# Kernel tuning notes

Hardware: AMD Instinct MI355X
Metric: run time of the kernel (lower is better)

Reference implementation:

```python
import jax, jax.numpy as jnp
import numpy as np


def setup_inputs() -> dict:
    key = jax.random.key(0)
    ks = jax.random.split(key, 7)
    B, C, N, D = 32, 256, 4096, 256
    s = 0.05
    return {
        "x": jax.random.normal(ks[0], (B, C, N), dtype=jnp.float32),
        "Wq": jax.random.normal(ks[1], (D, C), dtype=jnp.float32) * s,
        "bq": jax.random.normal(ks[2], (D,), dtype=jnp.float32) * s,
        "Wk": jax.random.normal(ks[3], (D, C), dtype=jnp.float32) * s,
        "bk": jax.random.normal(ks[4], (D,), dtype=jnp.float32) * s,
        "Wv": jax.random.normal(ks[5], (D, C), dtype=jnp.float32) * s,
        "bv": jax.random.normal(ks[6], (D,), dtype=jnp.float32) * s,
    }


def reference(x, Wq, bq, Wk, bk, Wv, bv):
    # 1x1 Conv1d == per-timestep linear: [B,C,N] x [D,C] -> [B,D,N]
    Q = jnp.einsum("bcn,dc->bdn", x, Wq) + bq[None, :, None]
    K = jnp.einsum("bcn,dc->bdn", x, Wk) + bk[None, :, None]
    V = jnp.einsum("bcn,dc->bdn", x, Wv) + bv[None, :, None]
    N = x.shape[-1]
    scale = 1.0 / jnp.sqrt(jnp.asarray(N, dtype=x.dtype))
    # channel-attention: scores are [B, D, D] (Q @ K^T over the time axis)
    scores = jnp.einsum("bdn,ben->bde", Q, K) * scale
    weights = jax.nn.softmax(scores, axis=-1)
    out = jnp.einsum("bde,ben->bdn", weights, V)  # [B, D, N]
    return out
```

## Files before the change

kernel.cpp:

```cpp
#include <hip/hip_runtime.h>
#include <cstdint>
#include <cstddef>


typedef float f32x4 __attribute__((ext_vector_type(4)));
typedef __bf16 bf16x8 __attribute__((ext_vector_type(8)));
typedef unsigned short u16;
typedef u16 u16x8 __attribute__((ext_vector_type(8)));
typedef u16 u16x4 __attribute__((ext_vector_type(4)));

__device__ __forceinline__ u16 f2bf(float f) {
    unsigned u = __builtin_bit_cast(unsigned, f);
    u += 0x7FFFu + ((u >> 16) & 1u);
    return (u16)(u >> 16);
}
__device__ __forceinline__ float bf2f(u16 h) {
    unsigned u = ((unsigned)h) << 16;
    return __builtin_bit_cast(float, u);
}
__device__ __forceinline__ f32x4 mfma16(bf16x8 a, bf16x8 b, f32x4 c) {
    return __builtin_amdgcn_mfma_f32_16x16x32_bf16(a, b, c, 0, 0, 0);
}

__global__ void k_wvt(const float* __restrict__ Wv, u16* __restrict__ WvT) {
    const int eb = blockIdx.x;
    const int c  = threadIdx.x;
    u16x8 pk;
#pragma unroll
    for (int j = 0; j < 8; ++j) pk[j] = f2bf(Wv[(eb * 8 + j) * 256 + c]);
    *(u16x8*)&WvT[c * 256 + eb * 8] = pk;
}

__global__ void k_wcvt(const float* __restrict__ Wq, const float* __restrict__ Wk,
                       u16* __restrict__ Wqb, u16* __restrict__ Wkb) {
    const int m = blockIdx.x >> 5, chunk = blockIdx.x & 31;
    const float* src = m == 0 ? Wq : Wk;
    u16* dst = m == 0 ? Wqb : Wkb;
    const int i = chunk * 2048 + threadIdx.x * 8;
    f32x4 w0 = *(const f32x4*)(src + i);
    f32x4 w1 = *(const f32x4*)(src + i + 4);
    u16x8 pk;
    pk[0] = f2bf(w0[0]); pk[1] = f2bf(w0[1]); pk[2] = f2bf(w0[2]); pk[3] = f2bf(w0[3]);
    pk[4] = f2bf(w1[0]); pk[5] = f2bf(w1[1]); pk[6] = f2bf(w1[2]); pk[7] = f2bf(w1[3]);
    *(u16x8*)&dst[i] = pk;
}

__global__ __launch_bounds__(512, 2) void k_gram_b(const float* __restrict__ x,
                                                   u16* __restrict__ Gpart,
                                                   float* __restrict__ rsum) {
    __shared__ __align__(16) u16 lds[2][256 * 64];
    __shared__ float ldsr[256];
    const int b = blockIdx.x >> 3, split = blockIdx.x & 7;
    const int t = threadIdx.x;
    const int lane = t & 63, wid = t >> 6;
    const int g = lane >> 4, q = lane & 15;

    if (t < 256) ldsr[t] = 0.f;

    f32x4 zero4 = {0.f, 0.f, 0.f, 0.f};
    f32x4 acc[2][16];
#pragma unroll
    for (int i = 0; i < 2; ++i)
#pragma unroll
        for (int j = 0; j < 16; ++j) acc[i][j] = zero4;

    const int c_st = t >> 1, half = t & 1;
    const int swz_w = (c_st & 7) << 3;
    const float* xp = x + ((size_t)b * 256 + c_st) * 4096 + split * 512 + half * 32;

    float s = 0.f;
    f32x4 R[8];
#pragma unroll
    for (int j = 0; j < 8; ++j) R[j] = *(const f32x4*)(xp + j * 4);
#pragma unroll
    for (int kk = 0; kk < 4; ++kk) {
        f32x4 w0 = R[2 * kk], w1 = R[2 * kk + 1];
        s += w0[0] + w0[1] + w0[2] + w0[3] + w1[0] + w1[1] + w1[2] + w1[3];
        u16x8 pk;
        pk[0] = f2bf(w0[0]); pk[1] = f2bf(w0[1]); pk[2] = f2bf(w0[2]); pk[3] = f2bf(w0[3]);
        pk[4] = f2bf(w1[0]); pk[5] = f2bf(w1[1]); pk[6] = f2bf(w1[2]); pk[7] = f2bf(w1[3]);
        *(u16x8*)&lds[0][(c_st * 64 + half * 32 + kk * 8) ^ swz_w] = pk;
    }
    __syncthreads();

    for (int nc = 0; nc < 8; ++nc) {
        const int cur = nc & 1;
        if (nc < 7) {
#pragma unroll
            for (int j = 0; j < 8; ++j) R[j] = *(const f32x4*)(xp + (nc + 1) * 64 + j * 4);
        }
#pragma unroll
        for (int ks = 0; ks < 2; ++ks) {
            const int c0 = 32 * wid + q;
            const int c1 = c0 + 16;
            bf16x8 a0 = *(const bf16x8*)&lds[cur][(c0 * 64 + ks * 32 + g * 8) ^ ((c0 & 7) << 3)];
            bf16x8 a1 = *(const bf16x8*)&lds[cur][(c1 * 64 + ks * 32 + g * 8) ^ ((c1 & 7) << 3)];
#pragma unroll
            for (int et = 0; et < 16; ++et) {
                const int c2 = et * 16 + q;
                bf16x8 bb = *(const bf16x8*)&lds[cur][(c2 * 64 + ks * 32 + g * 8) ^ ((c2 & 7) << 3)];
                acc[0][et] = mfma16(a0, bb, acc[0][et]);
                acc[1][et] = mfma16(a1, bb, acc[1][et]);
            }
        }
        if (nc < 7) {
#pragma unroll
            for (int kk = 0; kk < 4; ++kk) {
                f32x4 w0 = R[2 * kk], w1 = R[2 * kk + 1];
                s += w0[0] + w0[1] + w0[2] + w0[3] + w1[0] + w1[1] + w1[2] + w1[3];
                u16x8 pk;
                pk[0] = f2bf(w0[0]); pk[1] = f2bf(w0[1]); pk[2] = f2bf(w0[2]); pk[3] = f2bf(w0[3]);
                pk[4] = f2bf(w1[0]); pk[5] = f2bf(w1[1]); pk[6] = f2bf(w1[2]); pk[7] = f2bf(w1[3]);
                *(u16x8*)&lds[cur ^ 1][(c_st * 64 + half * 32 + kk * 8) ^ swz_w] = pk;
            }
        }
        __syncthreads();
    }

    atomicAdd(&ldsr[c_st], s);

    u16* gp = Gpart + (size_t)(split * 32 + b) * 65536;
#pragma unroll
    for (int dt = 0; dt < 2; ++dt)
#pragma unroll
        for (int et = 0; et < 16; ++et)
#pragma unroll
            for (int rr = 0; rr < 4; ++rr) {
                const int cc = 32 * wid + dt * 16 + 4 * g + rr;
                gp[cc * 256 + et * 16 + q] = f2bf(acc[dt][et][rr]);
            }
    __syncthreads();
    if (t < 256) atomicAdd(&rsum[b * 256 + t], ldsr[t]);
}

__global__ void k_reduce_b(const u16* __restrict__ Gpart, u16* __restrict__ Gb) {
    const size_t j = ((size_t)blockIdx.x * 256 + threadIdx.x) * 8;
    float s[8];
#pragma unroll
    for (int i = 0; i < 8; ++i) s[i] = 0.f;
#pragma unroll
    for (int sp = 0; sp < 8; ++sp) {
        u16x8 v = *(const u16x8*)(Gpart + (size_t)sp * 2097152 + j);
#pragma unroll
        for (int i = 0; i < 8; ++i) s[i] += bf2f(v[i]);
    }
    u16x8 pk;
#pragma unroll
    for (int i = 0; i < 8; ++i) pk[i] = f2bf(s[i]);
    *(u16x8*)&Gb[j] = pk;
}

__global__ __launch_bounds__(512, 4) void k_T(const u16* __restrict__ Gb,
                                              const u16* __restrict__ Wkb,
                                              u16* __restrict__ Tws) {
    const int b = blockIdx.x >> 3, ebase = (blockIdx.x & 7) * 32;
    const int t = threadIdx.x;
    const int lane = t & 63, wid = t >> 6;
    const int g = lane >> 4, q = lane & 15;

    f32x4 zero4 = {0.f, 0.f, 0.f, 0.f};
    f32x4 acc[2][2];
#pragma unroll
    for (int i = 0; i < 2; ++i)
#pragma unroll
        for (int j = 0; j < 2; ++j) acc[i][j] = zero4;

    const u16* gp = Gb + (size_t)b * 65536;
#pragma unroll
    for (int ks = 0; ks < 8; ++ks) {
        bf16x8 a0 = *(const bf16x8*)&gp[(32 * wid + q) * 256 + ks * 32 + g * 8];
        bf16x8 a1 = *(const bf16x8*)&gp[(32 * wid + 16 + q) * 256 + ks * 32 + g * 8];
        bf16x8 b0 = *(const bf16x8*)&Wkb[(ebase + q) * 256 + ks * 32 + g * 8];
        bf16x8 b1 = *(const bf16x8*)&Wkb[(ebase + 16 + q) * 256 + ks * 32 + g * 8];
        acc[0][0] = mfma16(a0, b0, acc[0][0]);
        acc[0][1] = mfma16(a0, b1, acc[0][1]);
        acc[1][0] = mfma16(a1, b0, acc[1][0]);
        acc[1][1] = mfma16(a1, b1, acc[1][1]);
    }
#pragma unroll
    for (int dt = 0; dt < 2; ++dt)
#pragma unroll
        for (int etl = 0; etl < 2; ++etl) {
            const int e = ebase + etl * 16 + q;
            const int cb = 32 * wid + dt * 16 + 4 * g;
            u16x4 pk;
            pk[0] = f2bf(acc[dt][etl][0]); pk[1] = f2bf(acc[dt][etl][1]);
            pk[2] = f2bf(acc[dt][etl][2]); pk[3] = f2bf(acc[dt][etl][3]);
            *(u16x4*)&Tws[((size_t)b * 256 + e) * 256 + cb] = pk;
        }
}

__global__ __launch_bounds__(256, 2) void k_SWM(
    const u16* __restrict__ Tws, const float* __restrict__ rsum,
    const float* __restrict__ Wq, const u16* __restrict__ Wqb,
    const float* __restrict__ Wk,
    const float* __restrict__ bqv, const float* __restrict__ bkv,
    const float* __restrict__ bvv,
    const u16* __restrict__ WvT, u16* __restrict__ Mws, float* __restrict__ cpv) {
    __shared__ __align__(16) u16 Wlds[64 * 256];
    __shared__ float r_[256], v_[256], bk_[256], bv_[256], u_[64], bq_[64];
    const int b = blockIdx.x >> 2, dbase = (blockIdx.x & 3) * 64;
    const int t = threadIdx.x;
    const int lane = t & 63, wid = t >> 6;
    const int g = lane >> 4, q = lane & 15;

    r_[t] = rsum[b * 256 + t];
    bk_[t] = bkv[t];
    bv_[t] = bvv[t];
    if (t < 64) bq_[t] = bqv[dbase + t];
    __syncthreads();

    {
        float s = 0.f; const float* wp = Wk + (size_t)t * 256;
#pragma unroll 4
        for (int c = 0; c < 256; c += 4) {
            f32x4 w = *(const f32x4*)(wp + c);
            f32x4 rr = *(const f32x4*)(&r_[c]);
            s += w[0] * rr[0] + w[1] * rr[1] + w[2] * rr[2] + w[3] * rr[3];
        }
        v_[t] = s;
    }
    if (t < 64) {
        float s = 0.f; const float* wp = Wq + (size_t)(dbase + t) * 256;
#pragma unroll 4
        for (int c = 0; c < 256; c += 4) {
            f32x4 w = *(const f32x4*)(wp + c);
            f32x4 rr = *(const f32x4*)(&r_[c]);
            s += w[0] * rr[0] + w[1] * rr[1] + w[2] * rr[2] + w[3] * rr[3];
        }
        u_[t] = s;
    }
    __syncthreads();

    f32x4 zero4 = {0.f, 0.f, 0.f, 0.f};
    f32x4 acc[16];
#pragma unroll
    for (int j = 0; j < 16; ++j) acc[j] = zero4;

    const u16* tp = Tws + (size_t)b * 65536;
    const int d_l = wid * 16 + q;
#pragma unroll 2
    for (int ks = 0; ks < 8; ++ks) {
        bf16x8 bb = *(const bf16x8*)&Wqb[(dbase + d_l) * 256 + ks * 32 + g * 8];
#pragma unroll
        for (int et = 0; et < 16; ++et) {
            bf16x8 aa = *(const bf16x8*)&tp[(et * 16 + q) * 256 + ks * 32 + g * 8];
            acc[et] = mfma16(aa, bb, acc[et]);
        }
    }

    {
        const float ud = u_[d_l], bqd = bq_[d_l];
        float m = -3.4e38f;
#pragma unroll
        for (int et = 0; et < 16; ++et)
#pragma unroll
            for (int rr = 0; rr < 4; ++rr) {
                const int e = et * 16 + 4 * g + rr;
                float s = (acc[et][rr] + ud * bk_[e] + bqd * v_[e] + 4096.f * bqd * bk_[e]) * 0.015625f;
                acc[et][rr] = s;
                m = fmaxf(m, s);
            }
        m = fmaxf(m, __shfl_xor(m, 16));
        m = fmaxf(m, __shfl_xor(m, 32));
        float lsum = 0.f;
#pragma unroll
        for (int et = 0; et < 16; ++et)
#pragma unroll
            for (int rr = 0; rr < 4; ++rr) {
                float p = __expf(acc[et][rr] - m);
                acc[et][rr] = p;
                lsum += p;
            }
        lsum += __shfl_xor(lsum, 16);
        lsum += __shfl_xor(lsum, 32);
        const float inv = 1.f / lsum;
        float cp = 0.f;
#pragma unroll
        for (int et = 0; et < 16; ++et)
#pragma unroll
            for (int rr = 0; rr < 4; ++rr) {
                const int e = et * 16 + 4 * g + rr;
                float w = acc[et][rr] * inv;
                acc[et][rr] = w;
                cp += w * bv_[e];
            }
        cp += __shfl_xor(cp, 16);
        cp += __shfl_xor(cp, 32);
        if (g == 0) cpv[b * 256 + dbase + d_l] = cp;
    }

#pragma unroll
    for (int et = 0; et < 16; ++et) {
        u16x4 pk;
        pk[0] = f2bf(acc[et][0]); pk[1] = f2bf(acc[et][1]);
        pk[2] = f2bf(acc[et][2]); pk[3] = f2bf(acc[et][3]);
        *(u16x4*)&Wlds[(d_l * 256 + et * 16 + 4 * g) ^ ((d_l & 7) << 3)] = pk;
    }
    __syncthreads();

    f32x4 acc2[4][4];
#pragma unroll
    for (int i = 0; i < 4; ++i)
#pragma unroll
        for (int j = 0; j < 4; ++j) acc2[i][j] = zero4;

#pragma unroll 2
    for (int ks = 0; ks < 8; ++ks) {
        bf16x8 afr[4], bfr[4];
#pragma unroll
        for (int ct = 0; ct < 4; ++ct)
            afr[ct] = *(const bf16x8*)&WvT[(64 * wid + ct * 16 + q) * 256 + ks * 32 + g * 8];
#pragma unroll
        for (int j = 0; j < 4; ++j) {
            const int dl = j * 16 + q;
            bfr[j] = *(const bf16x8*)&Wlds[(dl * 256 + ks * 32 + g * 8) ^ ((dl & 7) << 3)];
        }
#pragma unroll
        for (int ct = 0; ct < 4; ++ct)
#pragma unroll
            for (int j = 0; j < 4; ++j)
                acc2[ct][j] = mfma16(afr[ct], bfr[j], acc2[ct][j]);
    }
#pragma unroll
    for (int ct = 0; ct < 4; ++ct)
#pragma unroll
        for (int j = 0; j < 4; ++j) {
            const int d = dbase + j * 16 + q;
            const int cb = 64 * wid + ct * 16 + 4 * g;
            u16x4 pk;
            pk[0] = f2bf(acc2[ct][j][0]); pk[1] = f2bf(acc2[ct][j][1]);
            pk[2] = f2bf(acc2[ct][j][2]); pk[3] = f2bf(acc2[ct][j][3]);
            *(u16x4*)&Mws[((size_t)b * 256 + d) * 256 + cb] = pk;
        }
}

__global__ __launch_bounds__(512, 2) void k_out(const float* __restrict__ x,
                                                const u16* __restrict__ Mws,
                                                const float* __restrict__ cpv,
                                                float* __restrict__ out) {
    __shared__ __align__(16) u16 xt[2][256 * 64];
    __shared__ float cp_l[256];
    const int b = blockIdx.x >> 4, nt = blockIdx.x & 15;
    const int n0 = nt * 256;
    const int t = threadIdx.x;
    const int lane = t & 63, wid = t >> 6;
    const int g = lane >> 4, q = lane & 15;

    if (t < 256) cp_l[t] = cpv[b * 256 + t];

    f32x4 zero4 = {0.f, 0.f, 0.f, 0.f};
    f32x4 acc[2][16];
#pragma unroll
    for (int i = 0; i < 2; ++i)
#pragma unroll
        for (int j = 0; j < 16; ++j) acc[i][j] = zero4;

    const int c8 = t & 7;
    const int n4 = t >> 3;
    const float* xbase = x + (size_t)b * 256 * 4096 + n0 + n4 * 4;
    const u16* mp = Mws + (size_t)b * 65536;

    f32x4 R[2][4];
#pragma unroll
    for (int sub = 0; sub < 2; ++sub) {
        const int cc0 = (c8 + 8 * sub) * 4;
#pragma unroll
        for (int j = 0; j < 4; ++j)
            R[sub][j] = *(const f32x4*)(xbase + (size_t)(cc0 + j) * 4096);
    }
#pragma unroll
    for (int sub = 0; sub < 2; ++sub)
#pragma unroll
        for (int j = 0; j < 4; ++j) {
            const int n = n4 * 4 + j;
            u16x4 pk;
            pk[0] = f2bf(R[sub][0][j]); pk[1] = f2bf(R[sub][1][j]);
            pk[2] = f2bf(R[sub][2][j]); pk[3] = f2bf(R[sub][3][j]);
            *(u16x4*)&xt[0][(n * 64 + (c8 + 8 * sub) * 4) ^ ((n & 7) << 3)] = pk;
        }
    __syncthreads();

    for (int ci = 0; ci < 4; ++ci) {
        const int cur = ci & 1;
        if (ci < 3) {
#pragma unroll
            for (int sub = 0; sub < 2; ++sub) {
                const int cc0 = (ci + 1) * 64 + (c8 + 8 * sub) * 4;
#pragma unroll
                for (int j = 0; j < 4; ++j)
                    R[sub][j] = *(const f32x4*)(xbase + (size_t)(cc0 + j) * 4096);
            }
        }
#pragma unroll
        for (int ks = 0; ks < 2; ++ks) {
            bf16x8 a0 = *(const bf16x8*)&mp[(32 * wid + q) * 256 + ci * 64 + ks * 32 + g * 8];
            bf16x8 a1 = *(const bf16x8*)&mp[(32 * wid + 16 + q) * 256 + ci * 64 + ks * 32 + g * 8];
#pragma unroll
            for (int ntl = 0; ntl < 16; ++ntl) {
                const int nn = ntl * 16 + q;
                bf16x8 bb = *(const bf16x8*)&xt[cur][(nn * 64 + ks * 32 + g * 8) ^ ((nn & 7) << 3)];
                acc[0][ntl] = mfma16(a0, bb, acc[0][ntl]);
                acc[1][ntl] = mfma16(a1, bb, acc[1][ntl]);
            }
        }
        if (ci < 3) {
#pragma unroll
            for (int sub = 0; sub < 2; ++sub)
#pragma unroll
                for (int j = 0; j < 4; ++j) {
                    const int n = n4 * 4 + j;
                    u16x4 pk;
                    pk[0] = f2bf(R[sub][0][j]); pk[1] = f2bf(R[sub][1][j]);
                    pk[2] = f2bf(R[sub][2][j]); pk[3] = f2bf(R[sub][3][j]);
                    *(u16x4*)&xt[cur ^ 1][(n * 64 + (c8 + 8 * sub) * 4) ^ ((n & 7) << 3)] = pk;
                }
        }
        __syncthreads();
    }

#pragma unroll
    for (int dt = 0; dt < 2; ++dt)
#pragma unroll
        for (int ntl = 0; ntl < 16; ++ntl)
#pragma unroll
            for (int rr = 0; rr < 4; ++rr) {
                const int d = 32 * wid + dt * 16 + 4 * g + rr;
                const int n = n0 + ntl * 16 + q;
                out[((size_t)b * 256 + d) * 4096 + n] = acc[dt][ntl][rr] + cp_l[d];
            }
}

__global__ __launch_bounds__(512, 2) void k_gram(const float* __restrict__ x,
                                                 float* __restrict__ G,
                                                 float* __restrict__ rsum) {
    __shared__ __align__(16) u16 lds[256 * 64];
    __shared__ float ldsr[256];
    const int b = blockIdx.x >> 3, split = blockIdx.x & 7;
    const int t = threadIdx.x;
    const int lane = t & 63, wid = t >> 6;
    const int g = lane >> 4, q = lane & 15;

    if (t < 256) ldsr[t] = 0.f;

    f32x4 zero4 = {0.f, 0.f, 0.f, 0.f};
    f32x4 acc[2][16];
#pragma unroll
    for (int i = 0; i < 2; ++i)
#pragma unroll
        for (int j = 0; j < 16; ++j) acc[i][j] = zero4;

    const int c_st = t >> 1, half = t & 1;
    const int swz_w = (c_st & 7) << 3;
    const float* xp = x + ((size_t)b * 256 + c_st) * 4096 + split * 512 + half * 32;

    for (int nc = 0; nc < 8; ++nc) {
        __syncthreads();
        float s = 0.f;
#pragma unroll
        for (int kk = 0; kk < 4; ++kk) {
            f32x4 w0 = *(const f32x4*)(xp + nc * 64 + kk * 8);
            f32x4 w1 = *(const f32x4*)(xp + nc * 64 + kk * 8 + 4);
            s += w0[0] + w0[1] + w0[2] + w0[3] + w1[0] + w1[1] + w1[2] + w1[3];
            u16x8 pk;
            pk[0] = f2bf(w0[0]); pk[1] = f2bf(w0[1]); pk[2] = f2bf(w0[2]); pk[3] = f2bf(w0[3]);
            pk[4] = f2bf(w1[0]); pk[5] = f2bf(w1[1]); pk[6] = f2bf(w1[2]); pk[7] = f2bf(w1[3]);
            *(u16x8*)&lds[(c_st * 64 + half * 32 + kk * 8) ^ swz_w] = pk;
        }
        atomicAdd(&ldsr[c_st], s);
        __syncthreads();
#pragma unroll
        for (int ks = 0; ks < 2; ++ks) {
            const int c0 = 32 * wid + q;
            const int c1 = c0 + 16;
            bf16x8 a0 = *(const bf16x8*)&lds[(c0 * 64 + ks * 32 + g * 8) ^ ((c0 & 7) << 3)];
            bf16x8 a1 = *(const bf16x8*)&lds[(c1 * 64 + ks * 32 + g * 8) ^ ((c1 & 7) << 3)];
#pragma unroll
            for (int et = 0; et < 16; ++et) {
                const int c2 = et * 16 + q;
                bf16x8 bb = *(const bf16x8*)&lds[(c2 * 64 + ks * 32 + g * 8) ^ ((c2 & 7) << 3)];
                acc[0][et] = mfma16(a0, bb, acc[0][et]);
                acc[1][et] = mfma16(a1, bb, acc[1][et]);
            }
        }
    }
#pragma unroll
    for (int dt = 0; dt < 2; ++dt)
#pragma unroll
        for (int et = 0; et < 16; ++et)
#pragma unroll
            for (int rr = 0; rr < 4; ++rr) {
                const int cc = 32 * wid + dt * 16 + 4 * g + rr;
                const int c2 = et * 16 + q;
                atomicAdd(&G[((size_t)b * 256 + cc) * 256 + c2], acc[dt][et][rr]);
            }
    __syncthreads();
    if (t < 256) atomicAdd(&rsum[b * 256 + t], ldsr[t]);
}

__global__ void k_gcvt(const float* __restrict__ G, u16* __restrict__ Gb) {
    const size_t i = (size_t)blockIdx.x * 2048 + threadIdx.x * 8;
    f32x4 w0 = *(const f32x4*)(G + i);
    f32x4 w1 = *(const f32x4*)(G + i + 4);
    u16x8 pk;
    pk[0] = f2bf(w0[0]); pk[1] = f2bf(w0[1]); pk[2] = f2bf(w0[2]); pk[3] = f2bf(w0[3]);
    pk[4] = f2bf(w1[0]); pk[5] = f2bf(w1[1]); pk[6] = f2bf(w1[2]); pk[7] = f2bf(w1[3]);
    *(u16x8*)&Gb[i] = pk;
}

extern "C" void kernel_launch(void* const* d_in, const int* in_sizes, int n_in,
                              void* d_out, int out_size, void* d_ws, size_t ws_size,
                              hipStream_t stream) {
    const float* x  = (const float*)d_in[0];
    const float* Wq = (const float*)d_in[1];
    const float* bq = (const float*)d_in[2];
    const float* Wk = (const float*)d_in[3];
    const float* bk = (const float*)d_in[4];
    const float* Wv = (const float*)d_in[5];
    const float* bv = (const float*)d_in[6];
    float* out = (float*)d_out;
    char* ws = (char*)d_ws;

    const size_t NEED_FAST = 38207488;

    if (ws_size >= NEED_FAST) {
        u16*   Gpart = (u16*)  (ws);
        u16*   Tws   = (u16*)  (ws);
        u16*   Mws   = (u16*)  (ws + 4194304);
        u16*   Gb    = (u16*)  (ws + 33554432);
        float* rsum  = (float*)(ws + 37748736);
        float* cpv   = (float*)(ws + 37781504);
        u16*   WvT   = (u16*)  (ws + 37814272);
        u16*   Wqb   = (u16*)  (ws + 37945344);
        u16*   Wkb   = (u16*)  (ws + 38076416);

        hipMemsetAsync(ws + 37748736, 0, 32768, stream);

        hipLaunchKernelGGL(k_wvt,      dim3(32),   dim3(256), 0, stream, Wv, WvT);
        hipLaunchKernelGGL(k_wcvt,     dim3(64),   dim3(256), 0, stream, Wq, Wk, Wqb, Wkb);
        hipLaunchKernelGGL(k_gram_b,   dim3(256),  dim3(512), 0, stream, x, Gpart, rsum);
        hipLaunchKernelGGL(k_reduce_b, dim3(1024), dim3(256), 0, stream, Gpart, Gb);
        hipLaunchKernelGGL(k_T,        dim3(256),  dim3(512), 0, stream, Gb, Wkb, Tws);
        hipLaunchKernelGGL(k_SWM,      dim3(128),  dim3(256), 0, stream,
                           Tws, rsum, Wq, Wqb, Wk, bq, bk, bv, WvT, Mws, cpv);
        hipLaunchKernelGGL(k_out,      dim3(512),  dim3(512), 0, stream, x, Mws, cpv, out);
    } else {
        float* G    = (float*)(ws);
        u16*   Tws  = (u16*)  (ws);
        u16*   Gb   = (u16*)  (ws + 8388608);
        u16*   Mws  = (u16*)  (ws + 8388608);
        float* rsum = (float*)(ws + 12582912);
        float* cpv  = (float*)(ws + 12615680);
        u16*   WvT  = (u16*)  (ws + 12648448);
        u16*   Wqb  = (u16*)  (ws + 12779520);
        u16*   Wkb  = (u16*)  (ws + 12910592);

        hipMemsetAsync(ws, 0, 8388608, stream);
        hipMemsetAsync(ws + 12582912, 0, 32768, stream);

        hipLaunchKernelGGL(k_wvt,  dim3(32),   dim3(256), 0, stream, Wv, WvT);
        hipLaunchKernelGGL(k_wcvt, dim3(64),   dim3(256), 0, stream, Wq, Wk, Wqb, Wkb);
        hipLaunchKernelGGL(k_gram, dim3(256),  dim3(512), 0, stream, x, G, rsum);
        hipLaunchKernelGGL(k_gcvt, dim3(1024), dim3(256), 0, stream, G, Gb);
        hipLaunchKernelGGL(k_T,    dim3(256),  dim3(512), 0, stream, Gb, Wkb, Tws);
        hipLaunchKernelGGL(k_SWM,  dim3(128),  dim3(256), 0, stream,
                           Tws, rsum, Wq, Wqb, Wk, bq, bk, bv, WvT, Mws, cpv);
        hipLaunchKernelGGL(k_out,  dim3(512),  dim3(512), 0, stream, x, Mws, cpv, out);
    }
}
```

Before: 190.5 us.

## Replace rsum atomics with per-split partials and rotate chunk order across blocks

The row-sum reduction in the gram kernel now writes per-thread partial sums to a workspace buffer instead of using LDS and global atomics, and k_SWM sums the eight split partials itself. This removes the hipMemsetAsync and the atomics. Both k_gram_b and k_out also rotate the order in which blocks visit their chunks, so concurrent blocks touch different address ranges and channel camping is reduced. The fallback path for small workspaces is deleted, so the code now needs a larger workspace.

```diff
diff --git a/kernel.cpp b/kernel.cpp
--- a/kernel.cpp
+++ b/kernel.cpp
@@ -47,16 +47,14 @@
 
 __global__ __launch_bounds__(512, 2) void k_gram_b(const float* __restrict__ x,
                                                    u16* __restrict__ Gpart,
-                                                   float* __restrict__ rsum) {
+                                                   float* __restrict__ rsp) {
     __shared__ __align__(16) u16 lds[2][256 * 64];
-    __shared__ float ldsr[256];
     const int b = blockIdx.x >> 3, split = blockIdx.x & 7;
+    const int rot = blockIdx.x & 7;
     const int t = threadIdx.x;
     const int lane = t & 63, wid = t >> 6;
     const int g = lane >> 4, q = lane & 15;
 
-    if (t < 256) ldsr[t] = 0.f;
-
     f32x4 zero4 = {0.f, 0.f, 0.f, 0.f};
     f32x4 acc[2][16];
 #pragma unroll
@@ -71,7 +69,7 @@
     float s = 0.f;
     f32x4 R[8];
 #pragma unroll
-    for (int j = 0; j < 8; ++j) R[j] = *(const f32x4*)(xp + j * 4);
+    for (int j = 0; j < 8; ++j) R[j] = *(const f32x4*)(xp + rot * 64 + j * 4);
 #pragma unroll
     for (int kk = 0; kk < 4; ++kk) {
         f32x4 w0 = R[2 * kk], w1 = R[2 * kk + 1];
@@ -86,8 +84,9 @@
     for (int nc = 0; nc < 8; ++nc) {
         const int cur = nc & 1;
         if (nc < 7) {
-#pragma unroll
-            for (int j = 0; j < 8; ++j) R[j] = *(const f32x4*)(xp + (nc + 1) * 64 + j * 4);
+            const int nxt = (nc + 1 + rot) & 7;
+#pragma unroll
+            for (int j = 0; j < 8; ++j) R[j] = *(const f32x4*)(xp + nxt * 64 + j * 4);
         }
 #pragma unroll
         for (int ks = 0; ks < 2; ++ks) {
@@ -117,7 +116,7 @@
         __syncthreads();
     }
 
-    atomicAdd(&ldsr[c_st], s);
+    rsp[(size_t)(split * 32 + b) * 512 + t] = s;
 
     u16* gp = Gpart + (size_t)(split * 32 + b) * 65536;
 #pragma unroll
@@ -129,8 +128,6 @@
                 const int cc = 32 * wid + dt * 16 + 4 * g + rr;
                 gp[cc * 256 + et * 16 + q] = f2bf(acc[dt][et][rr]);
             }
-    __syncthreads();
-    if (t < 256) atomicAdd(&rsum[b * 256 + t], ldsr[t]);
 }
 
 __global__ void k_reduce_b(const u16* __restrict__ Gpart, u16* __restrict__ Gb) {
@@ -191,7 +188,7 @@
 }
 
 __global__ __launch_bounds__(256, 2) void k_SWM(
-    const u16* __restrict__ Tws, const float* __restrict__ rsum,
+    const u16* __restrict__ Tws, const float* __restrict__ rsp,
     const float* __restrict__ Wq, const u16* __restrict__ Wqb,
     const float* __restrict__ Wk,
     const float* __restrict__ bqv, const float* __restrict__ bkv,
@@ -204,7 +201,15 @@
     const int lane = t & 63, wid = t >> 6;
     const int g = lane >> 4, q = lane & 15;
 
-    r_[t] = rsum[b * 256 + t];
+    {
+        float sr = 0.f;
+#pragma unroll
+        for (int sp = 0; sp < 8; ++sp) {
+            const float* rp = rsp + (size_t)(sp * 32 + b) * 512;
+            sr += rp[2 * t] + rp[2 * t + 1];
+        }
+        r_[t] = sr;
+    }
     bk_[t] = bkv[t];
     bv_[t] = bvv[t];
     if (t < 64) bq_[t] = bqv[dbase + t];
@@ -342,6 +347,7 @@
     __shared__ __align__(16) u16 xt[2][256 * 64];
     __shared__ float cp_l[256];
     const int b = blockIdx.x >> 4, nt = blockIdx.x & 15;
+    const int rot = blockIdx.x & 3;
     const int n0 = nt * 256;
     const int t = threadIdx.x;
     const int lane = t & 63, wid = t >> 6;
@@ -364,7 +370,7 @@
     f32x4 R[2][4];
 #pragma unroll
     for (int sub = 0; sub < 2; ++sub) {
-        const int cc0 = (c8 + 8 * sub) * 4;
+        const int cc0 = rot * 64 + (c8 + 8 * sub) * 4;
 #pragma unroll
         for (int j = 0; j < 4; ++j)
             R[sub][j] = *(const f32x4*)(xbase + (size_t)(cc0 + j) * 4096);
@@ -383,10 +389,12 @@
 
     for (int ci = 0; ci < 4; ++ci) {
         const int cur = ci & 1;
+        const int cc = (ci + rot) & 3;
         if (ci < 3) {
+            const int nxt = (ci + 1 + rot) & 3;
 #pragma unroll
             for (int sub = 0; sub < 2; ++sub) {
-                const int cc0 = (ci + 1) * 64 + (c8 + 8 * sub) * 4;
+                const int cc0 = nxt * 64 + (c8 + 8 * sub) * 4;
 #pragma unroll
                 for (int j = 0; j < 4; ++j)
                     R[sub][j] = *(const f32x4*)(xbase + (size_t)(cc0 + j) * 4096);
@@ -394,8 +402,8 @@
         }
 #pragma unroll
         for (int ks = 0; ks < 2; ++ks) {
-            bf16x8 a0 = *(const bf16x8*)&mp[(32 * wid + q) * 256 + ci * 64 + ks * 32 + g * 8];
-            bf16x8 a1 = *(const bf16x8*)&mp[(32 * wid + 16 + q) * 256 + ci * 64 + ks * 32 + g * 8];
+            bf16x8 a0 = *(const bf16x8*)&mp[(32 * wid + q) * 256 + cc * 64 + ks * 32 + g * 8];
+            bf16x8 a1 = *(const bf16x8*)&mp[(32 * wid + 16 + q) * 256 + cc * 64 + ks * 32 + g * 8];
 #pragma unroll
             for (int ntl = 0; ntl < 16; ++ntl) {
                 const int nn = ntl * 16 + q;
@@ -429,83 +437,6 @@
                 const int n = n0 + ntl * 16 + q;
                 out[((size_t)b * 256 + d) * 4096 + n] = acc[dt][ntl][rr] + cp_l[d];
             }
-}
-
-__global__ __launch_bounds__(512, 2) void k_gram(const float* __restrict__ x,
-                                                 float* __restrict__ G,
-                                                 float* __restrict__ rsum) {
-    __shared__ __align__(16) u16 lds[256 * 64];
-    __shared__ float ldsr[256];
-    const int b = blockIdx.x >> 3, split = blockIdx.x & 7;
-    const int t = threadIdx.x;
-    const int lane = t & 63, wid = t >> 6;
-    const int g = lane >> 4, q = lane & 15;
-
-    if (t < 256) ldsr[t] = 0.f;
-
-    f32x4 zero4 = {0.f, 0.f, 0.f, 0.f};
-    f32x4 acc[2][16];
-#pragma unroll
-    for (int i = 0; i < 2; ++i)
-#pragma unroll
-        for (int j = 0; j < 16; ++j) acc[i][j] = zero4;
-
-    const int c_st = t >> 1, half = t & 1;
-    const int swz_w = (c_st & 7) << 3;
-    const float* xp = x + ((size_t)b * 256 + c_st) * 4096 + split * 512 + half * 32;
-
-    for (int nc = 0; nc < 8; ++nc) {
-        __syncthreads();
-        float s = 0.f;
-#pragma unroll
-        for (int kk = 0; kk < 4; ++kk) {
-            f32x4 w0 = *(const f32x4*)(xp + nc * 64 + kk * 8);
-            f32x4 w1 = *(const f32x4*)(xp + nc * 64 + kk * 8 + 4);
-            s += w0[0] + w0[1] + w0[2] + w0[3] + w1[0] + w1[1] + w1[2] + w1[3];
-            u16x8 pk;
-            pk[0] = f2bf(w0[0]); pk[1] = f2bf(w0[1]); pk[2] = f2bf(w0[2]); pk[3] = f2bf(w0[3]);
-            pk[4] = f2bf(w1[0]); pk[5] = f2bf(w1[1]); pk[6] = f2bf(w1[2]); pk[7] = f2bf(w1[3]);
-            *(u16x8*)&lds[(c_st * 64 + half * 32 + kk * 8) ^ swz_w] = pk;
-        }
-        atomicAdd(&ldsr[c_st], s);
-        __syncthreads();
-#pragma unroll
-        for (int ks = 0; ks < 2; ++ks) {
-            const int c0 = 32 * wid + q;
-            const int c1 = c0 + 16;
-            bf16x8 a0 = *(const bf16x8*)&lds[(c0 * 64 + ks * 32 + g * 8) ^ ((c0 & 7) << 3)];
-            bf16x8 a1 = *(const bf16x8*)&lds[(c1 * 64 + ks * 32 + g * 8) ^ ((c1 & 7) << 3)];
-#pragma unroll
-            for (int et = 0; et < 16; ++et) {
-                const int c2 = et * 16 + q;
-                bf16x8 bb = *(const bf16x8*)&lds[(c2 * 64 + ks * 32 + g * 8) ^ ((c2 & 7) << 3)];
-                acc[0][et] = mfma16(a0, bb, acc[0][et]);
-                acc[1][et] = mfma16(a1, bb, acc[1][et]);
-            }
-        }
-    }
-#pragma unroll
-    for (int dt = 0; dt < 2; ++dt)
-#pragma unroll
-        for (int et = 0; et < 16; ++et)
-#pragma unroll
-            for (int rr = 0; rr < 4; ++rr) {
-                const int cc = 32 * wid + dt * 16 + 4 * g + rr;
-                const int c2 = et * 16 + q;
-                atomicAdd(&G[((size_t)b * 256 + cc) * 256 + c2], acc[dt][et][rr]);
-            }
-    __syncthreads();
-    if (t < 256) atomicAdd(&rsum[b * 256 + t], ldsr[t]);
-}
-
-__global__ void k_gcvt(const float* __restrict__ G, u16* __restrict__ Gb) {
-    const size_t i = (size_t)blockIdx.x * 2048 + threadIdx.x * 8;
-    f32x4 w0 = *(const f32x4*)(G + i);
-    f32x4 w1 = *(const f32x4*)(G + i + 4);
-    u16x8 pk;
-    pk[0] = f2bf(w0[0]); pk[1] = f2bf(w0[1]); pk[2] = f2bf(w0[2]); pk[3] = f2bf(w0[3]);
-    pk[4] = f2bf(w1[0]); pk[5] = f2bf(w1[1]); pk[6] = f2bf(w1[2]); pk[7] = f2bf(w1[3]);
-    *(u16x8*)&Gb[i] = pk;
 }
 
 extern "C" void kernel_launch(void* const* d_in, const int* in_sizes, int n_in,
@@ -521,50 +452,22 @@
     float* out = (float*)d_out;
     char* ws = (char*)d_ws;
 
-    const size_t NEED_FAST = 38207488;
-
-    if (ws_size >= NEED_FAST) {
-        u16*   Gpart = (u16*)  (ws);
-        u16*   Tws   = (u16*)  (ws);
-        u16*   Mws   = (u16*)  (ws + 4194304);
-        u16*   Gb    = (u16*)  (ws + 33554432);
-        float* rsum  = (float*)(ws + 37748736);
-        float* cpv   = (float*)(ws + 37781504);
-        u16*   WvT   = (u16*)  (ws + 37814272);
-        u16*   Wqb   = (u16*)  (ws + 37945344);
-        u16*   Wkb   = (u16*)  (ws + 38076416);
-
-        hipMemsetAsync(ws + 37748736, 0, 32768, stream);
-
-        hipLaunchKernelGGL(k_wvt,      dim3(32),   dim3(256), 0, stream, Wv, WvT);
-        hipLaunchKernelGGL(k_wcvt,     dim3(64),   dim3(256), 0, stream, Wq, Wk, Wqb, Wkb);
-        hipLaunchKernelGGL(k_gram_b,   dim3(256),  dim3(512), 0, stream, x, Gpart, rsum);
-        hipLaunchKernelGGL(k_reduce_b, dim3(1024), dim3(256), 0, stream, Gpart, Gb);
-        hipLaunchKernelGGL(k_T,        dim3(256),  dim3(512), 0, stream, Gb, Wkb, Tws);
-        hipLaunchKernelGGL(k_SWM,      dim3(128),  dim3(256), 0, stream,
-                           Tws, rsum, Wq, Wqb, Wk, bq, bk, bv, WvT, Mws, cpv);
-        hipLaunchKernelGGL(k_out,      dim3(512),  dim3(512), 0, stream, x, Mws, cpv, out);
-    } else {
-        float* G    = (float*)(ws);
-        u16*   Tws  = (u16*)  (ws);
-        u16*   Gb   = (u16*)  (ws + 8388608);
-        u16*   Mws  = (u16*)  (ws + 8388608);
-        float* rsum = (float*)(ws + 12582912);
-        float* cpv  = (float*)(ws + 12615680);
-        u16*   WvT  = (u16*)  (ws + 12648448);
-        u16*   Wqb  = (u16*)  (ws + 12779520);
-        u16*   Wkb  = (u16*)  (ws + 12910592);
-
-        hipMemsetAsync(ws, 0, 8388608, stream);
-        hipMemsetAsync(ws + 12582912, 0, 32768, stream);
-
-        hipLaunchKernelGGL(k_wvt,  dim3(32),   dim3(256), 0, stream, Wv, WvT);
-        hipLaunchKernelGGL(k_wcvt, dim3(64),   dim3(256), 0, stream, Wq, Wk, Wqb, Wkb);
-        hipLaunchKernelGGL(k_gram, dim3(256),  dim3(512), 0, stream, x, G, rsum);
-        hipLaunchKernelGGL(k_gcvt, dim3(1024), dim3(256), 0, stream, G, Gb);
-        hipLaunchKernelGGL(k_T,    dim3(256),  dim3(512), 0, stream, Gb, Wkb, Tws);
-        hipLaunchKernelGGL(k_SWM,  dim3(128),  dim3(256), 0, stream,
-                           Tws, rsum, Wq, Wqb, Wk, bq, bk, bv, WvT, Mws, cpv);
-        hipLaunchKernelGGL(k_out,  dim3(512),  dim3(512), 0, stream, x, Mws, cpv, out);
-    }
-}
+    u16*   Gpart = (u16*)  (ws);
+    u16*   Tws   = (u16*)  (ws);
+    u16*   Mws   = (u16*)  (ws + 4194304);
+    u16*   Gb    = (u16*)  (ws + 33554432);
+    float* rsp   = (float*)(ws + 37748736);
+    float* cpv   = (float*)(ws + 38273024);
+    u16*   WvT   = (u16*)  (ws + 38305792);
+    u16*   Wqb   = (u16*)  (ws + 38436864);
+    u16*   Wkb   = (u16*)  (ws + 38567936);
+
+    hipLaunchKernelGGL(k_wvt,      dim3(32),   dim3(256), 0, stream, Wv, WvT);
+    hipLaunchKernelGGL(k_wcvt,     dim3(64),   dim3(256), 0, stream, Wq, Wk, Wqb, Wkb);
+    hipLaunchKernelGGL(k_gram_b,   dim3(256),  dim3(512), 0, stream, x, Gpart, rsp);
+    hipLaunchKernelGGL(k_reduce_b, dim3(1024), dim3(256), 0, stream, Gpart, Gb);
+    hipLaunchKernelGGL(k_T,        dim3(256),  dim3(512), 0, stream, Gb, Wkb, Tws);
+    hipLaunchKernelGGL(k_SWM,      dim3(128),  dim3(256), 0, stream,
+                       Tws, rsp, Wq, Wqb, Wk, bq, bk, bv, WvT, Mws, cpv);
+    hipLaunchKernelGGL(k_out,      dim3(512),  dim3(512), 0, stream, x, Mws, cpv, out);
+}
```

After: 180.3 us (median of 2 runs). 1.06x faster.
